# Kernel tuning notes

Hardware: AMD Instinct MI355X
Metric: run time of the kernel (lower is better)

The kernel has to match this reference:

```python
import jax, jax.numpy as jnp
import numpy as np

B, S, H = 2, 2048, 1024
E, K, I, IS = 8, 2, 1408, 2816

def setup_inputs() -> dict:
    key = jax.random.key(0)
    ks = jax.random.split(key, 9)
    sc = lambda fan_in: 1.0 / np.sqrt(fan_in)
    return {
        'hidden_states': jax.random.normal(ks[0], (B, S, H), jnp.float32),
        'gate_w': jax.random.normal(ks[1], (H, E), jnp.float32) * sc(H),
        'w_gate': jax.random.normal(ks[2], (E, H, I), jnp.float32) * sc(H),
        'w_up': jax.random.normal(ks[3], (E, H, I), jnp.float32) * sc(H),
        'w_down': jax.random.normal(ks[4], (E, I, H), jnp.float32) * sc(I),
        'sh_gate_w': jax.random.normal(ks[5], (H, IS), jnp.float32) * sc(H),
        'sh_up_w': jax.random.normal(ks[6], (H, IS), jnp.float32) * sc(H),
        'sh_down_w': jax.random.normal(ks[7], (IS, H), jnp.float32) * sc(IS),
        'sh_expert_gate_w': jax.random.normal(ks[8], (H, 1), jnp.float32) * sc(H),
        'top_k': K,
    }

def reference(hidden_states, gate_w, w_gate, w_up, w_down, sh_gate_w, sh_up_w, sh_down_w, sh_expert_gate_w, top_k):
    orig_shape = hidden_states.shape
    x = hidden_states.reshape(-1, orig_shape[-1])  # [T, H]
    T = x.shape[0]
    n_experts = gate_w.shape[1]
    # --- routing (matches _route_single_token, no expert_bias) ---
    logits = x @ gate_w                               # [T, E]
    topk_vals, topk_ids = jax.lax.top_k(logits, top_k)  # [T, K]
    topk_weights = jax.nn.softmax(topk_vals, axis=-1)   # [T, K]
    # dense routing matrix [T, E]; each token has K nonzeros
    route = jnp.zeros((T, n_experts), x.dtype).at[jnp.arange(T)[:, None], topk_ids].add(topk_weights)
    # --- expert SwiGLU FFNs, masked-combine over the fixed expert set ---
    out = jnp.zeros_like(x)
    for e in range(n_experts):
        h = jax.nn.silu(x @ w_gate[e]) * (x @ w_up[e])  # [T, I]
        out = out + route[:, e:e + 1] * (h @ w_down[e])
    # --- shared expert (always active) with sigmoid gate ---
    shared = (jax.nn.silu(x @ sh_gate_w) * (x @ sh_up_w)) @ sh_down_w
    shared = jax.nn.sigmoid(x @ sh_expert_gate_w) * shared
    out = out + shared
    return out.reshape(orig_shape)
```

## Files before the change

### kernel.cpp

```cpp
#include <hip/hip_runtime.h>
#include <hip/hip_bf16.h>

#define T_TOK 4096
#define HDIM  1024
#define NEXP  8
#define IDIM  1408
#define ISDIM 2816

typedef short bf16x8 __attribute__((ext_vector_type(8)));
typedef float f32x4  __attribute__((ext_vector_type(4)));
typedef unsigned short u16;
typedef unsigned short u16x4 __attribute__((ext_vector_type(4)));
typedef unsigned short u16x8 __attribute__((ext_vector_type(8)));

typedef __attribute__((address_space(1))) const void gvoid;
typedef __attribute__((address_space(3))) void lvoid;

__device__ __forceinline__ u16 f2bf(float f) {
    union { float f; unsigned u; } c; c.f = f;
    unsigned r = (c.u + 0x7FFFu + ((c.u >> 16) & 1u)) >> 16;
    return (u16)r;
}
__device__ __forceinline__ float bf2f(u16 v) {
    union { unsigned u; float f; } c; c.u = (unsigned)v << 16; return c.f;
}
__device__ __forceinline__ void glds16(const u16* g, u16* l) {
    __builtin_amdgcn_global_load_lds((gvoid*)g, (lvoid*)l, 16, 0, 0);
}

__global__ __launch_bounds__(256) void route_kernel(
    const float* __restrict__ X, const float* __restrict__ GW,
    const float* __restrict__ SEG,
    int* __restrict__ topk_e, float* __restrict__ topk_w,
    float* __restrict__ sgate)
{
    const int t = blockIdx.x * 4 + (threadIdx.x >> 6);
    const int lane = threadIdx.x & 63;
    float acc[NEXP];
    #pragma unroll
    for (int e = 0; e < NEXP; ++e) acc[e] = 0.f;
    float sacc = 0.f;
    const float* xr = X + (size_t)t * HDIM;
    for (int h = lane; h < HDIM; h += 64) {
        float xv = xr[h];
        f32x4 g0 = *(const f32x4*)(GW + (size_t)h * NEXP);
        f32x4 g1 = *(const f32x4*)(GW + (size_t)h * NEXP + 4);
        acc[0] += xv * g0[0]; acc[1] += xv * g0[1];
        acc[2] += xv * g0[2]; acc[3] += xv * g0[3];
        acc[4] += xv * g1[0]; acc[5] += xv * g1[1];
        acc[6] += xv * g1[2]; acc[7] += xv * g1[3];
        sacc += xv * SEG[h];
    }
    #pragma unroll
    for (int off = 32; off > 0; off >>= 1) {
        #pragma unroll
        for (int e = 0; e < NEXP; ++e) acc[e] += __shfl_down(acc[e], off);
        sacc += __shfl_down(sacc, off);
    }
    if (lane == 0) {
        int e0 = 0;
        #pragma unroll
        for (int e = 1; e < NEXP; ++e) if (acc[e] > acc[e0]) e0 = e;
        int e1 = (e0 == 0) ? 1 : 0;
        #pragma unroll
        for (int e = 0; e < NEXP; ++e)
            if (e != e0 && acc[e] > acc[e1]) e1 = e;
        float w0 = 1.f / (1.f + __expf(acc[e1] - acc[e0]));
        topk_e[t * 2]     = e0; topk_e[t * 2 + 1] = e1;
        topk_w[t * 2]     = w0; topk_w[t * 2 + 1] = 1.f - w0;
        sgate[t] = 1.f / (1.f + __expf(-sacc));
    }
}

__global__ __launch_bounds__(256) void hist_kernel(
    const int* __restrict__ topk_e, int* __restrict__ counts)
{
    __shared__ int h[NEXP];
    if (threadIdx.x < NEXP) h[threadIdx.x] = 0;
    __syncthreads();
    int i = blockIdx.x * 256 + threadIdx.x;
    atomicAdd(&h[topk_e[i]], 1);
    __syncthreads();
    if (threadIdx.x < NEXP) atomicAdd(&counts[threadIdx.x], h[threadIdx.x]);
}

__global__ void offsets_kernel(const int* __restrict__ counts,
                               int* __restrict__ seg_start,
                               int* __restrict__ cursors)
{
    if (threadIdx.x == 0) {
        int s = 0;
        for (int e = 0; e < NEXP; ++e) {
            seg_start[e] = s; cursors[e] = s; s += counts[e];
        }
    }
}

__global__ __launch_bounds__(256) void scatter_kernel(
    const int* __restrict__ topk_e,
    int* __restrict__ cursors, int* __restrict__ tok_ids,
    int* __restrict__ slot)
{
    const int i = blockIdx.x * 256 + threadIdx.x;
    const int lane = threadIdx.x & 63;
    const int e = topk_e[i];
    const unsigned long long lt = (1ull << lane) - 1ull;
    #pragma unroll
    for (int ex = 0; ex < NEXP; ++ex) {
        unsigned long long mask = __ballot(e == ex);
        if (mask == 0ull) continue;
        int cnt = __popcll(mask);
        int leader = __ffsll((long long)mask) - 1;
        int base_ = 0;
        if (lane == leader) base_ = atomicAdd(&cursors[ex], cnt);
        base_ = __shfl(base_, leader);
        if (e == ex) {
            int pos = base_ + __popcll(mask & lt);
            tok_ids[pos] = i >> 1;
            slot[i] = pos;
        }
    }
}

__global__ __launch_bounds__(256) void cvt_x_kernel(
    const float* __restrict__ in, u16* __restrict__ out, int n)
{
    int i = (blockIdx.x * 256 + threadIdx.x) * 8;
    if (i < n) {
        f32x4 a = *(const f32x4*)(in + i);
        f32x4 b = *(const f32x4*)(in + i + 4);
        u16x8 o;
        #pragma unroll
        for (int j = 0; j < 4; ++j) { o[j] = f2bf(a[j]); o[j + 4] = f2bf(b[j]); }
        *(u16x8*)(out + i) = o;
    }
}

__global__ __launch_bounds__(256) void transpose_cvt(
    const float* __restrict__ in0, const float* __restrict__ in1,
    u16* __restrict__ out, int K, int N, int split, int ilv)
{
    const int z = blockIdx.z;
    const int e = (z < split) ? z : z - split;
    const float* in = (z < split) ? (in0 + (size_t)z * K * N)
                                  : (in1 + (size_t)(z - split) * K * N);
    u16* o = ilv ? (out + (size_t)e * 2 * N * K)
                 : (out + (size_t)z * N * K);
    const int radd = ilv ? ((z < split) ? 0 : 16) : 0;

    __shared__ float tile[64][65];
    const int n0 = blockIdx.x * 64, k0 = blockIdx.y * 64;
    const int tx = threadIdx.x & 15;
    const int ty = threadIdx.x >> 4;

    #pragma unroll
    for (int p = 0; p < 4; ++p) {
        int k = ty + p * 16;
        f32x4 v = *(const f32x4*)(in + (size_t)(k0 + k) * N + n0 + tx * 4);
        *(f32x4*)&tile[k][tx * 4] = v;
    }
    __syncthreads();
    #pragma unroll
    for (int p = 0; p < 4; ++p) {
        int n = ty + p * 16;
        u16x4 w;
        #pragma unroll
        for (int j = 0; j < 4; ++j) w[j] = f2bf(tile[tx * 4 + j][n]);
        int R = n0 + n;
        int orow = ilv ? (((R >> 4) * 32) + (R & 15) + radd) : R;
        *(u16x4*)(o + (size_t)orow * K + k0 + tx * 4) = w;
    }
}


#define MFMA16(MB, AV, BV) \
    _Pragma("unroll") for (int m_ = 0; m_ < 4; ++m_) \
        _Pragma("unroll") for (int n_ = 0; n_ < 4; ++n_) \
            acc[(MB) + m_][n_] = __builtin_amdgcn_mfma_f32_16x16x32_bf16(AV[m_], BV[n_], acc[(MB) + m_][n_], 0, 0, 0);

#define COMP256(bufo) do { \
    bf16x8 av[4], bv[4]; \
    _Pragma("unroll") for (int m_ = 0; m_ < 4; ++m_) av[m_] = *(const bf16x8*)&As[(bufo) + aof + m_ * 1024]; \
    _Pragma("unroll") for (int n_ = 0; n_ < 4; ++n_) bv[n_] = *(const bf16x8*)&Bs[(bufo) + bof + n_ * 1024]; \
    __builtin_amdgcn_s_setprio(1); MFMA16(0, av, bv) __builtin_amdgcn_s_setprio(0); \
    _Pragma("unroll") for (int m_ = 0; m_ < 4; ++m_) av[m_] = *(const bf16x8*)&As[(bufo) + aof + (m_ + 4) * 1024]; \
    __builtin_amdgcn_s_setprio(1); MFMA16(4, av, bv) __builtin_amdgcn_s_setprio(0); \
    _Pragma("unroll") for (int m_ = 0; m_ < 4; ++m_) av[m_] = *(const bf16x8*)&As[(bufo) + (aof ^ 32) + m_ * 1024]; \
    _Pragma("unroll") for (int n_ = 0; n_ < 4; ++n_) bv[n_] = *(const bf16x8*)&Bs[(bufo) + (bof ^ 32) + n_ * 1024]; \
    __builtin_amdgcn_s_setprio(1); MFMA16(0, av, bv) __builtin_amdgcn_s_setprio(0); \
    _Pragma("unroll") for (int m_ = 0; m_ < 4; ++m_) av[m_] = *(const bf16x8*)&As[(bufo) + (aof ^ 32) + (m_ + 4) * 1024]; \
    __builtin_amdgcn_s_setprio(1); MFMA16(4, av, bv) __builtin_amdgcn_s_setprio(0); \
} while (0)

#define STAGE256() do { \
    glds16(ap0, &As[stbuf + tid * 8]); \
    glds16(ap1, &As[stbuf + 4096 + tid * 8]); \
    glds16(ap2, &As[stbuf + 8192 + tid * 8]); \
    glds16(ap3, &As[stbuf + 12288 + tid * 8]); \
    glds16(bp0, &Bs[stbuf + tid * 8]); \
    glds16(bp1, &Bs[stbuf + 4096 + tid * 8]); \
    glds16(bp2, &Bs[stbuf + 8192 + tid * 8]); \
    glds16(bp3, &Bs[stbuf + 12288 + tid * 8]); \
    ap0 += 64; ap1 += 64; ap2 += 64; ap3 += 64; \
    bp0 += 64; bp1 += 64; bp2 += 64; bp3 += 64; \
    stbuf ^= 16384; } while (0)

#define GEMM_LOOP(NT) \
    STAGE256(); STAGE256(); \
    _Pragma("unroll 1") \
    for (int t = 0; t < (NT) - 2; ++t) { \
        asm volatile("s_waitcnt vmcnt(8)" ::: "memory"); \
        __builtin_amdgcn_s_barrier(); \
        COMP256((t & 1) * 16384); \
        __builtin_amdgcn_s_barrier(); \
        STAGE256(); \
    } \
    asm volatile("s_waitcnt vmcnt(8)" ::: "memory"); \
    __builtin_amdgcn_s_barrier(); \
    COMP256(0); \
    asm volatile("s_waitcnt vmcnt(0)" ::: "memory"); \
    __builtin_amdgcn_s_barrier(); \
    COMP256(16384);

__global__ __launch_bounds__(512, 2) void gemm_gu(
    const u16* __restrict__ A, const u16* __restrict__ Bc_, size_t b_stride,
    u16* __restrict__ Hout,
    const int* __restrict__ a_ids, const int* __restrict__ seg_start,
    const int* __restrict__ counts, int Nout)
{
    extern __shared__ u16 lds[];
    u16* As = lds;
    u16* Bs = lds + 32768;

    int e, m0, cnt, base;
    if (counts) {
        e = blockIdx.x; m0 = blockIdx.y * 256;
        cnt = counts[e]; base = seg_start[e];
    } else {
        e = 0; m0 = (blockIdx.x * gridDim.y + blockIdx.y) * 256;
        cnt = T_TOK; base = 0;
    }
    if (m0 >= cnt) return;
    const u16* Bsrc = Bc_ + (size_t)e * b_stride;
    const int K = HDIM;
    const int n0e = blockIdx.z * 256;

    const int tid = threadIdx.x;
    const int srow = tid >> 3;
    const int sw = ((tid & 7) ^ (srow & 7)) * 8;

    const u16 *ap0, *ap1, *ap2, *ap3, *bp0, *bp1, *bp2, *bp3;
    {
        int r0 = m0 + srow;       if (r0 >= cnt) r0 = cnt - 1;
        int r1 = m0 + 64 + srow;  if (r1 >= cnt) r1 = cnt - 1;
        int r2 = m0 + 128 + srow; if (r2 >= cnt) r2 = cnt - 1;
        int r3 = m0 + 192 + srow; if (r3 >= cnt) r3 = cnt - 1;
        int g0 = a_ids ? a_ids[base + r0] : (base + r0);
        int g1 = a_ids ? a_ids[base + r1] : (base + r1);
        int g2 = a_ids ? a_ids[base + r2] : (base + r2);
        int g3 = a_ids ? a_ids[base + r3] : (base + r3);
        ap0 = A + (size_t)g0 * K + sw;
        ap1 = A + (size_t)g1 * K + sw;
        ap2 = A + (size_t)g2 * K + sw;
        ap3 = A + (size_t)g3 * K + sw;
        bp0 = Bsrc + (size_t)(n0e + srow) * K + sw;
        bp1 = Bsrc + (size_t)(n0e + 64 + srow) * K + sw;
        bp2 = Bsrc + (size_t)(n0e + 128 + srow) * K + sw;
        bp3 = Bsrc + (size_t)(n0e + 192 + srow) * K + sw;
    }
    int stbuf = 0;

    f32x4 acc[8][4];
    #pragma unroll
    for (int i = 0; i < 8; ++i)
        #pragma unroll
        for (int j = 0; j < 4; ++j) acc[i][j] = (f32x4){0.f, 0.f, 0.f, 0.f};

    const int lane = tid & 63;
    const int wv = tid >> 6;
    const int wr = wv >> 2;
    const int wn = wv & 3;
    const int lrow = lane & 15;
    const int kslot = lane >> 4;
    const int aof = (wr * 128 + lrow) * 64 + ((kslot ^ (lrow & 7)) * 8);
    const int bof = (wn * 64 + lrow) * 64 + ((kslot ^ (lrow & 7)) * 8);

    GEMM_LOOP(16)

    const int l4 = kslot * 4;
    #pragma unroll
    for (int mf = 0; mf < 8; ++mf)
        #pragma unroll
        for (int p = 0; p < 2; ++p) {
            f32x4 g = acc[mf][2 * p], u = acc[mf][2 * p + 1];
            int ci = blockIdx.z * 128 + (wn * 2 + p) * 16 + lrow;
            #pragma unroll
            for (int j = 0; j < 4; ++j) {
                int r = m0 + wr * 128 + mf * 16 + l4 + j;
                if (r < cnt) {
                    float hv = g[j] / (1.f + __expf(-g[j])) * u[j];
                    Hout[(size_t)(base + r) * Nout + ci] = f2bf(hv);
                }
            }
        }
}

__global__ __launch_bounds__(512, 2) void gemm_down(
    const u16* __restrict__ AE, const u16* __restrict__ AS,
    const u16* __restrict__ WDt, const u16* __restrict__ SDt,
    float* __restrict__ DexpO, float* __restrict__ OutS,
    const int* __restrict__ seg_start, const int* __restrict__ counts)
{
    extern __shared__ u16 lds[];
    u16* As = lds;
    u16* Bs = lds + 32768;

    const int zz = blockIdx.x;
    const bool shr = (zz >= 32);
    int n0, cnt, base, kst;
    size_t koff;
    const u16 *Asrc, *Bsrc;
    if (!shr) {
        int e = zz & 7;
        n0 = (zz >> 3) * 256;
        cnt = counts[e]; base = seg_start[e];
        Asrc = AE; Bsrc = WDt + (size_t)e * (HDIM * IDIM);
        kst = IDIM; koff = 0;
    } else {
        int idx = zz - 32;
        n0 = (idx & 3) * 256;
        cnt = T_TOK; base = 0;
        Asrc = AS; Bsrc = SDt;
        kst = ISDIM; koff = (size_t)(idx >> 2) * 1408;
    }
    const int m0 = blockIdx.y * 256;
    if (m0 >= cnt) return;

    const int tid = threadIdx.x;
    const int srow = tid >> 3;
    const int sw = ((tid & 7) ^ (srow & 7)) * 8;

    const u16 *ap0, *ap1, *ap2, *ap3, *bp0, *bp1, *bp2, *bp3;
    {
        int r0 = m0 + srow;       if (r0 >= cnt) r0 = cnt - 1;
        int r1 = m0 + 64 + srow;  if (r1 >= cnt) r1 = cnt - 1;
        int r2 = m0 + 128 + srow; if (r2 >= cnt) r2 = cnt - 1;
        int r3 = m0 + 192 + srow; if (r3 >= cnt) r3 = cnt - 1;
        ap0 = Asrc + (size_t)(base + r0) * kst + koff + sw;
        ap1 = Asrc + (size_t)(base + r1) * kst + koff + sw;
        ap2 = Asrc + (size_t)(base + r2) * kst + koff + sw;
        ap3 = Asrc + (size_t)(base + r3) * kst + koff + sw;
        bp0 = Bsrc + (size_t)(n0 + srow) * kst + koff + sw;
        bp1 = Bsrc + (size_t)(n0 + 64 + srow) * kst + koff + sw;
        bp2 = Bsrc + (size_t)(n0 + 128 + srow) * kst + koff + sw;
        bp3 = Bsrc + (size_t)(n0 + 192 + srow) * kst + koff + sw;
    }
    int stbuf = 0;

    f32x4 acc[8][4];
    #pragma unroll
    for (int i = 0; i < 8; ++i)
        #pragma unroll
        for (int j = 0; j < 4; ++j) acc[i][j] = (f32x4){0.f, 0.f, 0.f, 0.f};

    const int lane = tid & 63;
    const int wv = tid >> 6;
    const int wr = wv >> 2;
    const int wn = wv & 3;
    const int lrow = lane & 15;
    const int kslot = lane >> 4;
    const int aof = (wr * 128 + lrow) * 64 + ((kslot ^ (lrow & 7)) * 8);
    const int bof = (wn * 64 + lrow) * 64 + ((kslot ^ (lrow & 7)) * 8);

    GEMM_LOOP(22)

    const int l4 = kslot * 4;
    #pragma unroll
    for (int mf = 0; mf < 8; ++mf)
        #pragma unroll
        for (int nf = 0; nf < 4; ++nf)
            #pragma unroll
            for (int j = 0; j < 4; ++j) {
                int r = m0 + wr * 128 + mf * 16 + l4 + j;
                if (r < cnt) {
                    int c = n0 + wn * 64 + nf * 16 + lrow;
                    if (!shr)
                        DexpO[(size_t)(base + r) * HDIM + c] = acc[mf][nf][j];
                    else
                        atomicAdd(&OutS[(size_t)r * HDIM + c], acc[mf][nf][j]);
                }
            }
}

__global__ __launch_bounds__(256) void combine_kernel(
    const float* __restrict__ Dexp,
    const int* __restrict__ slot, const float* __restrict__ topk_w,
    const float* __restrict__ sgate, float* __restrict__ Out)
{
    int idx = blockIdx.x * 256 + threadIdx.x;
    int t = idx >> 8;
    int c = (idx & 255) * 4;
    int s0 = slot[2 * t], s1 = slot[2 * t + 1];
    float w0 = topk_w[2 * t], w1 = topk_w[2 * t + 1], sg = sgate[t];
    f32x4 sh = *(const f32x4*)(Out + (size_t)t * HDIM + c);
    f32x4 d0 = *(const f32x4*)(Dexp + (size_t)s0 * HDIM + c);
    f32x4 d1 = *(const f32x4*)(Dexp + (size_t)s1 * HDIM + c);
    f32x4 o;
    #pragma unroll
    for (int j = 0; j < 4; ++j) o[j] = sg * sh[j] + w0 * d0[j] + w1 * d1[j];
    *(f32x4*)(Out + (size_t)t * HDIM + c) = o;
}

extern "C" void kernel_launch(void* const* d_in, const int* in_sizes, int n_in,
                              void* d_out, int out_size, void* d_ws, size_t ws_size,
                              hipStream_t stream)
{
    const float* X   = (const float*)d_in[0];
    const float* GW  = (const float*)d_in[1];
    const float* WG  = (const float*)d_in[2];
    const float* WU  = (const float*)d_in[3];
    const float* WD  = (const float*)d_in[4];
    const float* SG  = (const float*)d_in[5];
    const float* SU  = (const float*)d_in[6];
    const float* SD  = (const float*)d_in[7];
    const float* SEG = (const float*)d_in[8];
    float* Out = (float*)d_out;

    char* ws = (char*)d_ws;
    int*   counts    = (int*)(ws + 0);
    int*   seg_start = (int*)(ws + 64);
    int*   cursors   = (int*)(ws + 128);
    int*   topk_e    = (int*)(ws + 1024);
    float* topk_w    = (float*)(ws + 1024 + 32768);
    float* sgate     = (float*)(ws + 1024 + 65536);
    int*   tok_ids   = (int*)(ws + 1024 + 65536 + 16384);
    int*   slot      = (int*)(ws + 1024 + 65536 + 16384 + 32768);

    u16* Xbf  = (u16*)(ws + 0x40000ull);
    u16* Hact = (u16*)(ws + 0xA00000ull);
    u16* Hs   = (u16*)(ws + 0x2200000ull);
    u16* WGUc = (u16*)(ws + 0x3A00000ull);
    u16* WDt  = (u16*)(ws + 0x6900000ull);
    u16* SGUc = (u16*)(ws + 0x8100000ull);
    u16* SDt  = (u16*)(ws + 0x8D00000ull);
    float* Dexp = (float*)(ws + 0x3A00000ull);

    hipMemsetAsync(counts, 0, 64, stream);
    hipMemsetAsync(Out, 0, (size_t)T_TOK * HDIM * sizeof(float), stream);

    route_kernel<<<T_TOK / 4, 256, 0, stream>>>(X, GW, SEG, topk_e, topk_w, sgate);
    hist_kernel<<<(T_TOK * 2) / 256, 256, 0, stream>>>(topk_e, counts);
    offsets_kernel<<<1, 64, 0, stream>>>(counts, seg_start, cursors);
    scatter_kernel<<<(T_TOK * 2) / 256, 256, 0, stream>>>(topk_e, cursors, tok_ids, slot);

    cvt_x_kernel<<<(T_TOK * HDIM) / (256 * 8), 256, 0, stream>>>(X, Xbf, T_TOK * HDIM);
    transpose_cvt<<<dim3(IDIM / 64, HDIM / 64, 2 * NEXP), 256, 0, stream>>>(WG, WU, WGUc, HDIM, IDIM, NEXP, 1);
    transpose_cvt<<<dim3(HDIM / 64, IDIM / 64, NEXP), 256, 0, stream>>>(WD, WD, WDt, IDIM, HDIM, NEXP, 0);
    transpose_cvt<<<dim3(ISDIM / 64, HDIM / 64, 2), 256, 0, stream>>>(SG, SU, SGUc, HDIM, ISDIM, 1, 1);
    transpose_cvt<<<dim3(HDIM / 64, ISDIM / 64, 1), 256, 0, stream>>>(SD, SD, SDt, ISDIM, HDIM, 1, 0);

    gemm_gu<<<dim3(NEXP, 16, 11), 512, 131072, stream>>>(
        Xbf, WGUc, (size_t)2 * IDIM * HDIM, Hact,
        tok_ids, seg_start, counts, IDIM);
    gemm_gu<<<dim3(8, 2, 22), 512, 131072, stream>>>(
        Xbf, SGUc, 0, Hs,
        nullptr, nullptr, nullptr, ISDIM);

    gemm_down<<<dim3(40, 16), 512, 131072, stream>>>(
        Hact, Hs, WDt, SDt, Dexp, Out,
        seg_start, counts);

    combine_kernel<<<(T_TOK * HDIM / 4) / 256, 256, 0, stream>>>(
        Dexp, slot, topk_w, sgate, Out);
}
```

Baseline: 363.2 us.

## Interleave half-tile staging with MFMA compute and merge expert/shared gate-up launches

Rewrites the GEMM main loop so each K-tile is split into two halves, with global-to-LDS loads for the next tile issued between MFMA groups and finer barriers/waitcnts. This is meant to overlap memory traffic with compute instead of staging a full tile after compute. It drops the XOR swizzle and uses a 32-element row stride in LDS, which may introduce bank conflicts. The routed-expert and shared-expert gate/up GEMMs are also merged into one launch with a flat block index, removing a launch and letting both workloads share the GPU.

```diff
diff --git a/kernel.cpp b/kernel.cpp
--- a/kernel.cpp
+++ b/kernel.cpp
@@ -173,102 +173,108 @@
 }
 
 
-#define MFMA16(MB, AV, BV) \
-    _Pragma("unroll") for (int m_ = 0; m_ < 4; ++m_) \
-        _Pragma("unroll") for (int n_ = 0; n_ < 4; ++n_) \
-            acc[(MB) + m_][n_] = __builtin_amdgcn_mfma_f32_16x16x32_bf16(AV[m_], BV[n_], acc[(MB) + m_][n_], 0, 0, 0);
-
-#define COMP256(bufo) do { \
-    bf16x8 av[4], bv[4]; \
-    _Pragma("unroll") for (int m_ = 0; m_ < 4; ++m_) av[m_] = *(const bf16x8*)&As[(bufo) + aof + m_ * 1024]; \
-    _Pragma("unroll") for (int n_ = 0; n_ < 4; ++n_) bv[n_] = *(const bf16x8*)&Bs[(bufo) + bof + n_ * 1024]; \
-    __builtin_amdgcn_s_setprio(1); MFMA16(0, av, bv) __builtin_amdgcn_s_setprio(0); \
-    _Pragma("unroll") for (int m_ = 0; m_ < 4; ++m_) av[m_] = *(const bf16x8*)&As[(bufo) + aof + (m_ + 4) * 1024]; \
-    __builtin_amdgcn_s_setprio(1); MFMA16(4, av, bv) __builtin_amdgcn_s_setprio(0); \
-    _Pragma("unroll") for (int m_ = 0; m_ < 4; ++m_) av[m_] = *(const bf16x8*)&As[(bufo) + (aof ^ 32) + m_ * 1024]; \
-    _Pragma("unroll") for (int n_ = 0; n_ < 4; ++n_) bv[n_] = *(const bf16x8*)&Bs[(bufo) + (bof ^ 32) + n_ * 1024]; \
-    __builtin_amdgcn_s_setprio(1); MFMA16(0, av, bv) __builtin_amdgcn_s_setprio(0); \
-    _Pragma("unroll") for (int m_ = 0; m_ < 4; ++m_) av[m_] = *(const bf16x8*)&As[(bufo) + (aof ^ 32) + (m_ + 4) * 1024]; \
-    __builtin_amdgcn_s_setprio(1); MFMA16(4, av, bv) __builtin_amdgcn_s_setprio(0); \
-} while (0)
-
-#define STAGE256() do { \
-    glds16(ap0, &As[stbuf + tid * 8]); \
-    glds16(ap1, &As[stbuf + 4096 + tid * 8]); \
-    glds16(ap2, &As[stbuf + 8192 + tid * 8]); \
-    glds16(ap3, &As[stbuf + 12288 + tid * 8]); \
-    glds16(bp0, &Bs[stbuf + tid * 8]); \
-    glds16(bp1, &Bs[stbuf + 4096 + tid * 8]); \
-    glds16(bp2, &Bs[stbuf + 8192 + tid * 8]); \
-    glds16(bp3, &Bs[stbuf + 12288 + tid * 8]); \
-    ap0 += 64; ap1 += 64; ap2 += 64; ap3 += 64; \
-    bp0 += 64; bp1 += 64; bp2 += 64; bp3 += 64; \
-    stbuf ^= 16384; } while (0)
-
-#define GEMM_LOOP(NT) \
-    STAGE256(); STAGE256(); \
+#define BAR() __builtin_amdgcn_s_barrier()
+#define WCNT(n) asm volatile("s_waitcnt vmcnt(" #n ")" ::: "memory")
+
+#define GSTAGE_KH0(wb) \
+    glds16(aLo, &As[(wb) + tid * 8]); \
+    glds16(aHi, &As[(wb) + 4096 + tid * 8]); \
+    glds16(bLo, &Bs[(wb) + tid * 8]); \
+    glds16(bHi, &Bs[(wb) + 4096 + tid * 8]);
+#define GSTAGE_KH1(wb) \
+    glds16(aLo + 32, &As[(wb) + 8192 + tid * 8]); \
+    glds16(aHi + 32, &As[(wb) + 8192 + 4096 + tid * 8]); \
+    glds16(bLo + 32, &Bs[(wb) + 8192 + tid * 8]); \
+    glds16(bHi + 32, &Bs[(wb) + 8192 + 4096 + tid * 8]);
+
+#define RD_A(rb, kh, j0) \
+    _Pragma("unroll") for (int q = 0; q < 4; ++q) \
+        av[q] = *(const bf16x8*)&As[(rb) + (kh) * 8192 + aofs[(j0) + q]];
+#define RD_B(rb, kh) \
+    _Pragma("unroll") for (int q = 0; q < 4; ++q) \
+        bv[q] = *(const bf16x8*)&Bs[(rb) + (kh) * 8192 + bofs[q]];
+#define MF16(ms) \
+    __builtin_amdgcn_s_setprio(1); \
+    _Pragma("unroll") for (int q = 0; q < 4; ++q) \
+        _Pragma("unroll") for (int w = 0; w < 4; ++w) \
+            acc[(ms) + q][w] = __builtin_amdgcn_mfma_f32_16x16x32_bf16(av[q], bv[w], acc[(ms) + q][w], 0, 0, 0); \
+    __builtin_amdgcn_s_setprio(0);
+
+#define GEMM_MAIN(NT) \
+    GSTAGE_KH0(0) GSTAGE_KH1(0) \
+    aLo += 64; aHi += 64; bLo += 64; bHi += 64; \
+    WCNT(4); BAR(); \
     _Pragma("unroll 1") \
-    for (int t = 0; t < (NT) - 2; ++t) { \
-        asm volatile("s_waitcnt vmcnt(8)" ::: "memory"); \
-        __builtin_amdgcn_s_barrier(); \
-        COMP256((t & 1) * 16384); \
-        __builtin_amdgcn_s_barrier(); \
-        STAGE256(); \
+    for (int t = 0; t < (NT) - 1; ++t) { \
+        const int rb = (t & 1) * 16384, wb = rb ^ 16384; \
+        bf16x8 av[4], bv[4]; \
+        RD_A(rb, 0, 0) RD_B(rb, 0) \
+        GSTAGE_KH0(wb) \
+        BAR(); MF16(0) BAR(); \
+        RD_A(rb, 0, 4) \
+        GSTAGE_KH1(wb) \
+        BAR(); MF16(4) WCNT(8); BAR(); \
+        RD_A(rb, 1, 0) RD_B(rb, 1) \
+        BAR(); MF16(0) BAR(); \
+        RD_A(rb, 1, 4) \
+        BAR(); MF16(4) WCNT(4); BAR(); \
+        aLo += 64; aHi += 64; bLo += 64; bHi += 64; \
     } \
-    asm volatile("s_waitcnt vmcnt(8)" ::: "memory"); \
-    __builtin_amdgcn_s_barrier(); \
-    COMP256(0); \
-    asm volatile("s_waitcnt vmcnt(0)" ::: "memory"); \
-    __builtin_amdgcn_s_barrier(); \
-    COMP256(16384);
+    { \
+        const int rb = (((NT) - 1) & 1) * 16384; \
+        bf16x8 av[4], bv[4]; \
+        RD_A(rb, 0, 0) RD_B(rb, 0) \
+        BAR(); MF16(0) BAR(); \
+        RD_A(rb, 0, 4) \
+        BAR(); MF16(4) WCNT(0); BAR(); \
+        RD_A(rb, 1, 0) RD_B(rb, 1) \
+        BAR(); MF16(0) BAR(); \
+        RD_A(rb, 1, 4) \
+        BAR(); MF16(4) \
+    }
 
 __global__ __launch_bounds__(512, 2) void gemm_gu(
-    const u16* __restrict__ A, const u16* __restrict__ Bc_, size_t b_stride,
-    u16* __restrict__ Hout,
+    const u16* __restrict__ A,
+    const u16* __restrict__ WGUc, const u16* __restrict__ SGUc,
+    u16* __restrict__ HoutE, u16* __restrict__ HoutS,
     const int* __restrict__ a_ids, const int* __restrict__ seg_start,
-    const int* __restrict__ counts, int Nout)
+    const int* __restrict__ counts)
 {
     extern __shared__ u16 lds[];
     u16* As = lds;
     u16* Bs = lds + 32768;
 
-    int e, m0, cnt, base;
-    if (counts) {
-        e = blockIdx.x; m0 = blockIdx.y * 256;
+    const int zz = blockIdx.x;
+    int cnt, base, n0c, N, nblk;
+    const u16* Bsrc;
+    u16* Hout;
+    const int* ids;
+    if (zz < 88) {
+        int e = zz & 7;
+        nblk = zz >> 3;
         cnt = counts[e]; base = seg_start[e];
+        Bsrc = WGUc + (size_t)e * (2 * IDIM * HDIM);
+        Hout = HoutE; N = IDIM; ids = a_ids;
     } else {
-        e = 0; m0 = (blockIdx.x * gridDim.y + blockIdx.y) * 256;
+        nblk = zz - 88;
         cnt = T_TOK; base = 0;
-    }
+        Bsrc = SGUc; Hout = HoutS; N = ISDIM; ids = nullptr;
+    }
+    n0c = nblk * 256;
+    const int m0 = blockIdx.y * 256;
     if (m0 >= cnt) return;
-    const u16* Bsrc = Bc_ + (size_t)e * b_stride;
-    const int K = HDIM;
-    const int n0e = blockIdx.z * 256;
 
     const int tid = threadIdx.x;
-    const int srow = tid >> 3;
-    const int sw = ((tid & 7) ^ (srow & 7)) * 8;
-
-    const u16 *ap0, *ap1, *ap2, *ap3, *bp0, *bp1, *bp2, *bp3;
-    {
-        int r0 = m0 + srow;       if (r0 >= cnt) r0 = cnt - 1;
-        int r1 = m0 + 64 + srow;  if (r1 >= cnt) r1 = cnt - 1;
-        int r2 = m0 + 128 + srow; if (r2 >= cnt) r2 = cnt - 1;
-        int r3 = m0 + 192 + srow; if (r3 >= cnt) r3 = cnt - 1;
-        int g0 = a_ids ? a_ids[base + r0] : (base + r0);
-        int g1 = a_ids ? a_ids[base + r1] : (base + r1);
-        int g2 = a_ids ? a_ids[base + r2] : (base + r2);
-        int g3 = a_ids ? a_ids[base + r3] : (base + r3);
-        ap0 = A + (size_t)g0 * K + sw;
-        ap1 = A + (size_t)g1 * K + sw;
-        ap2 = A + (size_t)g2 * K + sw;
-        ap3 = A + (size_t)g3 * K + sw;
-        bp0 = Bsrc + (size_t)(n0e + srow) * K + sw;
-        bp1 = Bsrc + (size_t)(n0e + 64 + srow) * K + sw;
-        bp2 = Bsrc + (size_t)(n0e + 128 + srow) * K + sw;
-        bp3 = Bsrc + (size_t)(n0e + 192 + srow) * K + sw;
-    }
-    int stbuf = 0;
+    const int srow = tid >> 2;
+    const int sk = (tid & 3) * 8;
+    int rlo = m0 + srow;       if (rlo >= cnt) rlo = cnt - 1;
+    int rhi = m0 + 128 + srow; if (rhi >= cnt) rhi = cnt - 1;
+    const int glo = ids ? ids[base + rlo] : (base + rlo);
+    const int ghi = ids ? ids[base + rhi] : (base + rhi);
+    const u16* aLo = A + (size_t)glo * HDIM + sk;
+    const u16* aHi = A + (size_t)ghi * HDIM + sk;
+    const u16* bLo = Bsrc + (size_t)(n0c + srow) * HDIM + sk;
+    const u16* bHi = Bsrc + (size_t)(n0c + 128 + srow) * HDIM + sk;
 
     f32x4 acc[8][4];
     #pragma unroll
@@ -280,29 +286,40 @@
     const int wv = tid >> 6;
     const int wr = wv >> 2;
     const int wn = wv & 3;
-    const int lrow = lane & 15;
-    const int kslot = lane >> 4;
-    const int aof = (wr * 128 + lrow) * 64 + ((kslot ^ (lrow & 7)) * 8);
-    const int bof = (wn * 64 + lrow) * 64 + ((kslot ^ (lrow & 7)) * 8);
-
-    GEMM_LOOP(16)
-
-    const int l4 = kslot * 4;
-    #pragma unroll
-    for (int mf = 0; mf < 8; ++mf)
+    const int l15 = lane & 15;
+    const int ksl = lane >> 4;
+    int aofs[8], bofs[4];
+    #pragma unroll
+    for (int j = 0; j < 8; ++j) {
+        int mrow = (j >> 2) * 128 + wr * 64 + (j & 3) * 16;
+        aofs[j] = (mrow + l15) * 32 + ksl * 8;
+    }
+    #pragma unroll
+    for (int i = 0; i < 4; ++i) {
+        int nrow = (i >> 1) * 128 + wn * 32 + (i & 1) * 16;
+        bofs[i] = (nrow + l15) * 32 + ksl * 8;
+    }
+
+    GEMM_MAIN(16)
+
+    const int l4 = ksl * 4;
+    #pragma unroll
+    for (int j = 0; j < 8; ++j) {
+        int mrow = (j >> 2) * 128 + wr * 64 + (j & 3) * 16;
         #pragma unroll
         for (int p = 0; p < 2; ++p) {
-            f32x4 g = acc[mf][2 * p], u = acc[mf][2 * p + 1];
-            int ci = blockIdx.z * 128 + (wn * 2 + p) * 16 + lrow;
+            f32x4 g = acc[j][2 * p], u = acc[j][2 * p + 1];
+            int c = nblk * 128 + (p * 4 + wn) * 16 + l15;
             #pragma unroll
-            for (int j = 0; j < 4; ++j) {
-                int r = m0 + wr * 128 + mf * 16 + l4 + j;
+            for (int jj = 0; jj < 4; ++jj) {
+                int r = m0 + mrow + l4 + jj;
                 if (r < cnt) {
-                    float hv = g[j] / (1.f + __expf(-g[j])) * u[j];
-                    Hout[(size_t)(base + r) * Nout + ci] = f2bf(hv);
+                    float hv = g[jj] / (1.f + __expf(-g[jj])) * u[jj];
+                    Hout[(size_t)(base + r) * N + c] = f2bf(hv);
                 }
             }
         }
+    }
 }
 
 __global__ __launch_bounds__(512, 2) void gemm_down(
@@ -337,25 +354,14 @@
     if (m0 >= cnt) return;
 
     const int tid = threadIdx.x;
-    const int srow = tid >> 3;
-    const int sw = ((tid & 7) ^ (srow & 7)) * 8;
-
-    const u16 *ap0, *ap1, *ap2, *ap3, *bp0, *bp1, *bp2, *bp3;
-    {
-        int r0 = m0 + srow;       if (r0 >= cnt) r0 = cnt - 1;
-        int r1 = m0 + 64 + srow;  if (r1 >= cnt) r1 = cnt - 1;
-        int r2 = m0 + 128 + srow; if (r2 >= cnt) r2 = cnt - 1;
-        int r3 = m0 + 192 + srow; if (r3 >= cnt) r3 = cnt - 1;
-        ap0 = Asrc + (size_t)(base + r0) * kst + koff + sw;
-        ap1 = Asrc + (size_t)(base + r1) * kst + koff + sw;
-        ap2 = Asrc + (size_t)(base + r2) * kst + koff + sw;
-        ap3 = Asrc + (size_t)(base + r3) * kst + koff + sw;
-        bp0 = Bsrc + (size_t)(n0 + srow) * kst + koff + sw;
-        bp1 = Bsrc + (size_t)(n0 + 64 + srow) * kst + koff + sw;
-        bp2 = Bsrc + (size_t)(n0 + 128 + srow) * kst + koff + sw;
-        bp3 = Bsrc + (size_t)(n0 + 192 + srow) * kst + koff + sw;
-    }
-    int stbuf = 0;
+    const int srow = tid >> 2;
+    const int sk = (tid & 3) * 8;
+    int rlo = m0 + srow;       if (rlo >= cnt) rlo = cnt - 1;
+    int rhi = m0 + 128 + srow; if (rhi >= cnt) rhi = cnt - 1;
+    const u16* aLo = Asrc + (size_t)(base + rlo) * kst + koff + sk;
+    const u16* aHi = Asrc + (size_t)(base + rhi) * kst + koff + sk;
+    const u16* bLo = Bsrc + (size_t)(n0 + srow) * kst + koff + sk;
+    const u16* bHi = Bsrc + (size_t)(n0 + 128 + srow) * kst + koff + sk;
 
     f32x4 acc[8][4];
     #pragma unroll
@@ -367,29 +373,42 @@
     const int wv = tid >> 6;
     const int wr = wv >> 2;
     const int wn = wv & 3;
-    const int lrow = lane & 15;
-    const int kslot = lane >> 4;
-    const int aof = (wr * 128 + lrow) * 64 + ((kslot ^ (lrow & 7)) * 8);
-    const int bof = (wn * 64 + lrow) * 64 + ((kslot ^ (lrow & 7)) * 8);
-
-    GEMM_LOOP(22)
-
-    const int l4 = kslot * 4;
-    #pragma unroll
-    for (int mf = 0; mf < 8; ++mf)
-        #pragma unroll
-        for (int nf = 0; nf < 4; ++nf)
+    const int l15 = lane & 15;
+    const int ksl = lane >> 4;
+    int aofs[8], bofs[4];
+    #pragma unroll
+    for (int j = 0; j < 8; ++j) {
+        int mrow = (j >> 2) * 128 + wr * 64 + (j & 3) * 16;
+        aofs[j] = (mrow + l15) * 32 + ksl * 8;
+    }
+    #pragma unroll
+    for (int i = 0; i < 4; ++i) {
+        int nrow = (i >> 1) * 128 + wn * 32 + (i & 1) * 16;
+        bofs[i] = (nrow + l15) * 32 + ksl * 8;
+    }
+
+    GEMM_MAIN(22)
+
+    const int l4 = ksl * 4;
+    #pragma unroll
+    for (int j = 0; j < 8; ++j) {
+        int mrow = (j >> 2) * 128 + wr * 64 + (j & 3) * 16;
+        #pragma unroll
+        for (int i = 0; i < 4; ++i) {
+            int nrow = (i >> 1) * 128 + wn * 32 + (i & 1) * 16;
+            int c = n0 + nrow + l15;
             #pragma unroll
-            for (int j = 0; j < 4; ++j) {
-                int r = m0 + wr * 128 + mf * 16 + l4 + j;
+            for (int jj = 0; jj < 4; ++jj) {
+                int r = m0 + mrow + l4 + jj;
                 if (r < cnt) {
-                    int c = n0 + wn * 64 + nf * 16 + lrow;
                     if (!shr)
-                        DexpO[(size_t)(base + r) * HDIM + c] = acc[mf][nf][j];
+                        DexpO[(size_t)(base + r) * HDIM + c] = acc[j][i][jj];
                     else
-                        atomicAdd(&OutS[(size_t)r * HDIM + c], acc[mf][nf][j]);
+                        atomicAdd(&OutS[(size_t)r * HDIM + c], acc[j][i][jj]);
                 }
             }
+        }
+    }
 }
 
 __global__ __launch_bounds__(256) void combine_kernel(
@@ -459,12 +478,9 @@
     transpose_cvt<<<dim3(ISDIM / 64, HDIM / 64, 2), 256, 0, stream>>>(SG, SU, SGUc, HDIM, ISDIM, 1, 1);
     transpose_cvt<<<dim3(HDIM / 64, ISDIM / 64, 1), 256, 0, stream>>>(SD, SD, SDt, ISDIM, HDIM, 1, 0);
 
-    gemm_gu<<<dim3(NEXP, 16, 11), 512, 131072, stream>>>(
-        Xbf, WGUc, (size_t)2 * IDIM * HDIM, Hact,
-        tok_ids, seg_start, counts, IDIM);
-    gemm_gu<<<dim3(8, 2, 22), 512, 131072, stream>>>(
-        Xbf, SGUc, 0, Hs,
-        nullptr, nullptr, nullptr, ISDIM);
+    gemm_gu<<<dim3(110, 16), 512, 131072, stream>>>(
+        Xbf, WGUc, SGUc, Hact, Hs,
+        tok_ids, seg_start, counts);
 
     gemm_down<<<dim3(40, 16), 512, 131072, stream>>>(
         Hact, Hs, WDt, SDt, Dexp, Out,
```

Result: no change. 357.8 us (-1.5%).
